# Performance work log

Hardware: AMD Instinct MI355X
Metric: run time of the kernel (lower is better)

Reference implementation:

```python
import jax, jax.numpy as jnp
import numpy as np

N = 50000
E = 1600000
IN_DIM = 128
HID = 32
HEADS = 4
OUT = 32
NEG_SLOPE = 0.2


def gat_conv(h, src, dst, W, al, ar, b, n_heads, d_out):
    # h: [N, F_in]; W: [F_in, H*D]; al/ar: [H, D]; b: [H*D]
    n = h.shape[0]
    z = (h @ W).reshape(n, n_heads, d_out)            # [N,H,D]
    el = (z * al[None]).sum(-1)                        # [N,H]
    er = (z * ar[None]).sum(-1)                        # [N,H]
    e = el[src] + er[dst]                              # [E,H]
    e = jnp.where(e > 0, e, NEG_SLOPE * e)             # leaky_relu(0.2)
    # edge softmax grouped by destination node
    m = jax.ops.segment_max(e, dst, num_segments=n)    # [N,H]
    ex = jnp.exp(e - m[dst])                           # [E,H]
    s = jax.ops.segment_sum(ex, dst, num_segments=n)   # [N,H]
    alpha = ex / s[dst]                                # [E,H]
    msg = alpha[:, :, None] * z[src]                   # [E,H,D]
    out = jax.ops.segment_sum(msg, dst, num_segments=n)  # [N,H,D]
    return out + b.reshape(1, n_heads, d_out)


def setup_inputs() -> dict:
    key = jax.random.key(0)
    ks = jax.random.split(key, 12)
    h = jax.random.normal(ks[0], (N, IN_DIM), dtype=jnp.float32)
    src = jax.random.randint(ks[1], (E,), 0, N, dtype=jnp.int32)
    dst = jax.random.randint(ks[2], (E,), 0, N, dtype=jnp.int32)
    s1 = 1.0 / np.sqrt(IN_DIM)
    W1 = jax.random.uniform(ks[3], (IN_DIM, HEADS * HID), jnp.float32, -s1, s1)
    al1 = jax.random.normal(ks[4], (HEADS, HID), jnp.float32) * 0.1
    ar1 = jax.random.normal(ks[5], (HEADS, HID), jnp.float32) * 0.1
    b1 = jnp.zeros((HEADS * HID,), jnp.float32)
    f2 = HEADS * HID
    s2 = 1.0 / np.sqrt(f2)
    W2 = jax.random.uniform(ks[6], (f2, OUT), jnp.float32, -s2, s2)
    al2 = jax.random.normal(ks[7], (1, OUT), jnp.float32) * 0.1
    ar2 = jax.random.normal(ks[8], (1, OUT), jnp.float32) * 0.1
    b2 = jnp.zeros((OUT,), jnp.float32)
    return {"h": h, "src": src, "dst": dst, "W1": W1, "al1": al1, "ar1": ar1,
            "b1": b1, "W2": W2, "al2": al2, "ar2": ar2, "b2": b2}


def reference(h, src, dst, W1, al1, ar1, b1, W2, al2, ar2, b2):
    x = gat_conv(h, src, dst, W1, al1, ar1, b1, HEADS, HID)  # [N,H,D]
    x = x.reshape(N, HEADS * HID)                             # flatten(1)
    x = jax.nn.elu(x)                                         # act
    y = gat_conv(x, src, dst, W2, al2, ar2, b2, 1, OUT)       # [N,1,OUT]
    return y.squeeze(1)                                        # [N,OUT]
```

## Files before the change

kernel.cpp:

```cpp
#include <hip/hip_runtime.h>
#include <hip/hip_fp16.h>

#define NN 50000
#define NEG_SLOPE 0.2f
#define BSHIFT 9
#define BNODES (1 << BSHIFT)
#define NBUCK ((NN + BNODES - 1) >> BSHIFT)
#define BCAP 18432

typedef _Float16 f16x4 __attribute__((ext_vector_type(4)));
typedef _Float16 f16x8 __attribute__((ext_vector_type(8)));
typedef float    f32x4 __attribute__((ext_vector_type(4)));

__global__ void zero_kernel(unsigned* bucket_cursor, int* src_sorted_pad) {
    int i = threadIdx.x;
    if (i < NBUCK) bucket_cursor[i] = (unsigned)(i * BCAP);
    if (i < 64) src_sorted_pad[i] = 0;
}

__global__ __launch_bounds__(1024) void bucketA(
        const int* __restrict__ src, const int* __restrict__ dst,
        unsigned* __restrict__ bucket_cursor, int2* __restrict__ ebuf, int E) {
    __shared__ unsigned hist[NBUCK];
    int tid = threadIdx.x;
    if (tid < NBUCK) hist[tid] = 0u;
    __syncthreads();
    int e = blockIdx.x * 1024 + tid;
    int s = 0, d = 0, b = 0;
    bool valid = e < E;
    if (valid) {
        s = src[e]; d = dst[e]; b = d >> BSHIFT;
        atomicAdd(&hist[b], 1u);
    }
    __syncthreads();
    if (tid < NBUCK) {
        unsigned c = hist[tid];
        hist[tid] = c ? atomicAdd(&bucket_cursor[tid], c) : 0u;
    }
    __syncthreads();
    if (valid) {
        unsigned slot = atomicAdd(&hist[b], 1u);
        ebuf[slot] = make_int2(s, d);
    }
}

__global__ __launch_bounds__(512) void gemm1_mfma(
        const float* __restrict__ h, const float* __restrict__ W1,
        const float* __restrict__ al1, const float* __restrict__ ar1,
        __half* __restrict__ z1h, float* __restrict__ el1, float* __restrict__ er1, int N) {
    __shared__ alignas(16) __half hA[128 * 128];
    __shared__ alignas(16) __half Bt[128 * 128];
    int tid = threadIdx.x;
    int lane = tid & 63, w = tid >> 6;
    int row0 = blockIdx.x * 128;
    int nrow = min(128, N - row0);

    for (int idx = tid; idx < 128 * 32; idx += 512) {
        int row = idx >> 5, kq = idx & 31;
        float4 v = (row < nrow) ? ((const float4*)(h + (size_t)(row0 + row) * 128))[kq]
                                : make_float4(0.f, 0.f, 0.f, 0.f);
        f16x4 hv;
        hv[0] = (_Float16)v.x; hv[1] = (_Float16)v.y;
        hv[2] = (_Float16)v.z; hv[3] = (_Float16)v.w;
        int off = row * 256 + ((kq * 8) ^ ((row & 15) << 4));
        *(f16x4*)((char*)hA + off) = hv;
    }
    {
        int col = tid & 127, kg = tid >> 7;
        #pragma unroll
        for (int it = 0; it < 4; ++it) {
            int k0 = it * 32 + kg * 8;
            f16x8 wv;
            #pragma unroll
            for (int i = 0; i < 8; ++i)
                wv[i] = (_Float16)W1[(size_t)(k0 + i) * 128 + col];
            int off = col * 256 + ((k0 * 2) ^ ((col & 15) << 4));
            *(f16x8*)((char*)Bt + off) = wv;
        }
    }
    __syncthreads();

    f32x4 acc[8];
    #pragma unroll
    for (int ct = 0; ct < 8; ++ct) acc[ct] = (f32x4){0.f, 0.f, 0.f, 0.f};

    int arow = w * 16 + (lane & 15);
    int kbyte_lane = ((lane >> 4) * 8) * 2;
    #pragma unroll
    for (int ks = 0; ks < 4; ++ks) {
        int kb = ks * 64 + kbyte_lane;
        f16x8 a = *(const f16x8*)((const char*)hA + arow * 256 + (kb ^ ((arow & 15) << 4)));
        #pragma unroll
        for (int ct = 0; ct < 8; ++ct) {
            int col = ct * 16 + (lane & 15);
            f16x8 b = *(const f16x8*)((const char*)Bt + col * 256 + (kb ^ ((col & 15) << 4)));
            acc[ct] = __builtin_amdgcn_mfma_f32_16x16x32_f16(a, b, acc[ct], 0, 0, 0);
        }
    }

    int lrow = (lane >> 4) * 4;
    #pragma unroll
    for (int ct = 0; ct < 8; ++ct) {
        int col = ct * 16 + (lane & 15);
        #pragma unroll
        for (int r = 0; r < 4; ++r) {
            int rl = w * 16 + lrow + r;
            if (rl < nrow)
                z1h[(size_t)(row0 + rl) * 128 + col] = __float2half(acc[ct][r]);
        }
    }
    #pragma unroll
    for (int hh = 0; hh < 4; ++hh) {
        int c0 = hh * 32 + (lane & 15);
        float a_l0 = al1[c0], a_l1 = al1[c0 + 16];
        float a_r0 = ar1[c0], a_r1 = ar1[c0 + 16];
        #pragma unroll
        for (int r = 0; r < 4; ++r) {
            float v0 = acc[2 * hh][r], v1 = acc[2 * hh + 1][r];
            float pl = v0 * a_l0 + v1 * a_l1;
            float pr = v0 * a_r0 + v1 * a_r1;
            #pragma unroll
            for (int o = 8; o; o >>= 1) {
                pl += __shfl_xor(pl, o, 16);
                pr += __shfl_xor(pr, o, 16);
            }
            int rl = w * 16 + lrow + r;
            if ((lane & 15) == 0 && rl < nrow) {
                el1[(row0 + rl) * 4 + hh] = pl;
                er1[(row0 + rl) * 4 + hh] = pr;
            }
        }
    }
}

__global__ __launch_bounds__(1024) void scatterC(
        const int2* __restrict__ ebuf, const unsigned* __restrict__ bucket_cursor,
        unsigned* __restrict__ off, int* __restrict__ src_sorted, int N, int E) {
    __shared__ unsigned hist[BNODES], nodeoff[BNODES], wsum[8], bsz[128];
    int b = blockIdx.x, tid = threadIdx.x;
    int base = b << BSHIFT;
    unsigned rs = (unsigned)(b * BCAP), re = bucket_cursor[b];

    if (tid < 128) bsz[tid] = (tid < NBUCK) ? bucket_cursor[tid] - (unsigned)(tid * BCAP) : 0u;
    if (tid < BNODES) hist[tid] = 0u;
    __syncthreads();
    if (tid == 0) {
        unsigned r = 0;
        for (int t = 0; t < NBUCK; ++t) { unsigned c = bsz[t]; bsz[t] = r; r += c; }
        if (b == 0) off[N] = (unsigned)E;
    }
    __syncthreads();
    unsigned boff = bsz[b];

    for (unsigned i = rs + tid; i < re; i += 1024)
        atomicAdd(&hist[ebuf[i].y - base], 1u);
    __syncthreads();
    unsigned v = 0, x = 0;
    int lane = tid & 63, wv = tid >> 6;
    if (tid < BNODES) {
        v = hist[tid]; x = v;
        #pragma unroll
        for (int o = 1; o < 64; o <<= 1) {
            unsigned n = __shfl_up(x, o, 64);
            if (lane >= o) x += n;
        }
        if (lane == 63) wsum[wv] = x;
    }
    __syncthreads();
    if (tid == 0) {
        unsigned r = 0;
        #pragma unroll
        for (int k = 0; k < 8; ++k) { unsigned t = wsum[k]; wsum[k] = r; r += t; }
    }
    __syncthreads();
    if (tid < BNODES) {
        unsigned exoff = x - v + wsum[wv] + boff;
        nodeoff[tid] = exoff;
        if (base + tid < N) off[base + tid] = exoff;
        hist[tid] = 0u;
    }
    __syncthreads();
    for (unsigned i = rs + tid; i < re; i += 1024) {
        int2 ed = ebuf[i];
        int ln = ed.y - base;
        unsigned r = atomicAdd(&hist[ln], 1u);
        src_sorted[nodeoff[ln] + r] = ed.x;
    }
}

__global__ __launch_bounds__(256) void agg1_spmm(
        const int* __restrict__ src_sorted, const unsigned* __restrict__ off,
        const float* __restrict__ el1, const float* __restrict__ er1,
        const __half* __restrict__ z1h, const float* __restrict__ b1, __half* __restrict__ x) {
    int tid = threadIdx.x, lane = tid & 63, w = tid >> 6;
    int node = blockIdx.x * 4 + w;
    int start = (int)off[node], end = (int)off[node + 1];
    int g = lane >> 4, l16 = lane & 15, head = l16 >> 2;
    const char* zbase = (const char*)z1h + (unsigned)(l16 * 16);
    float er_d = er1[node * 4 + head];

    float acc[8];
    #pragma unroll
    for (int jj = 0; jj < 8; ++jj) acc[jj] = 0.f;
    float sloc = 0.f;
    for (int base = start; base < end; base += 32) {
        #pragma unroll
        for (int t = 0; t < 8; ++t) {
            int i = base + 4 * t + g;
            int s = src_sorted[i];
            float el = el1[(unsigned)s * 4u + head];
            float v = el + er_d;
            v = fmaxf(v, NEG_SLOPE * v);
            float ex = __expf(v);
            ex = (i < end) ? ex : 0.f;
            sloc += ex;
            float4 r = *(const float4*)(zbase + ((unsigned)s << 8));
            const __half* zh = (const __half*)&r;
            #pragma unroll
            for (int k = 0; k < 8; ++k)
                acc[k] = fmaf(__half2float(zh[k]), ex, acc[k]);
        }
    }
    #pragma unroll
    for (int jj = 0; jj < 8; ++jj) {
        acc[jj] += __shfl_xor(acc[jj], 16, 64);
        acc[jj] += __shfl_xor(acc[jj], 32, 64);
    }
    sloc += __shfl_xor(sloc, 16, 64);
    sloc += __shfl_xor(sloc, 32, 64);
    float inv = sloc > 0.f ? 1.f / sloc : 0.f;

    if (g == 0) {
        float xv[8];
        #pragma unroll
        for (int jj = 0; jj < 8; ++jj) {
            float t = acc[jj] * inv + b1[l16 * 8 + jj];
            xv[jj] = t > 0.f ? t : (__expf(t) - 1.f);
        }
        union { __half2 h2[4]; uint4 u; } pk;
        #pragma unroll
        for (int k = 0; k < 4; ++k) pk.h2[k] = __floats2half2_rn(xv[2 * k], xv[2 * k + 1]);
        *(uint4*)(x + ((size_t)node << 7) + l16 * 8) = pk.u;
    }
}

__global__ __launch_bounds__(256) void gemm2el_kernel(
        const __half* __restrict__ x, const float* __restrict__ W2,
        const float* __restrict__ al2, const float* __restrict__ ar2,
        __half* __restrict__ z2h, float* __restrict__ el2, float* __restrict__ er2, int N) {
    __shared__ __half xsh[64][136];
    __shared__ float W2T[32][132];
    int tid = threadIdx.x;
    int row0 = blockIdx.x * 64;
    int nrow = min(64, N - row0);

    for (int idx = tid; idx < nrow * 16; idx += 256) {
        int r = idx >> 4, kq = idx & 15;
        float4 v = ((const float4*)(x + (size_t)(row0 + r) * 128))[kq];
        *(float4*)&xsh[r][kq * 8] = v;
    }
    for (int idx = tid; idx < 4096; idx += 256) {
        int k = idx >> 5, c = idx & 31;
        W2T[c][k] = W2[idx];
    }
    __syncthreads();

    int gc = tid & 15, gr = tid >> 4;
    float acc[4][2];
    #pragma unroll
    for (int j = 0; j < 4; ++j) { acc[j][0] = 0.f; acc[j][1] = 0.f; }

    for (int p = 0; p < 32; ++p) {
        float4 w0 = *(const float4*)&W2T[gc][p * 4];
        float4 w1 = *(const float4*)&W2T[gc + 16][p * 4];
        #pragma unroll
        for (int j = 0; j < 4; ++j) {
            const __half* xr = &xsh[gr * 4 + j][p * 4];
            float x0 = __half2float(xr[0]), x1 = __half2float(xr[1]);
            float x2 = __half2float(xr[2]), x3 = __half2float(xr[3]);
            acc[j][0] = fmaf(x0, w0.x, fmaf(x1, w0.y, fmaf(x2, w0.z, fmaf(x3, w0.w, acc[j][0]))));
            acc[j][1] = fmaf(x0, w1.x, fmaf(x1, w1.y, fmaf(x2, w1.z, fmaf(x3, w1.w, acc[j][1]))));
        }
    }

    float al0 = al2[gc], al1v = al2[gc + 16];
    float ar0 = ar2[gc], ar1v = ar2[gc + 16];
    #pragma unroll
    for (int j = 0; j < 4; ++j) {
        int r = gr * 4 + j;
        int node = row0 + r;
        bool live = r < nrow;
        if (live) {
            z2h[(size_t)node * 32 + gc]      = __float2half(acc[j][0]);
            z2h[(size_t)node * 32 + gc + 16] = __float2half(acc[j][1]);
        }
        float pl = acc[j][0] * al0 + acc[j][1] * al1v;
        float pr = acc[j][0] * ar0 + acc[j][1] * ar1v;
        #pragma unroll
        for (int o = 8; o; o >>= 1) {
            pl += __shfl_xor(pl, o, 16);
            pr += __shfl_xor(pr, o, 16);
        }
        if (live && gc == 0) { el2[node] = pl; er2[node] = pr; }
    }
}

__global__ __launch_bounds__(256) void agg2_fused(
        const int* __restrict__ src_sorted, const unsigned* __restrict__ off,
        const float* __restrict__ el2, const float* __restrict__ er2,
        const __half* __restrict__ z2h, const float* __restrict__ b2,
        float* __restrict__ out) {
    int tid = threadIdx.x, lane = tid & 63;
    int node = blockIdx.x * 4 + (tid >> 6);
    int start = (int)off[node], end = (int)off[node + 1];
    float er_d = er2[node];

    int g = lane >> 2, l4 = lane & 3;
    const char* zbase = (const char*)z2h + (unsigned)(l4 * 16);
    float acc[8];
    #pragma unroll
    for (int jj = 0; jj < 8; ++jj) acc[jj] = 0.f;
    float sloc = 0.f;
    for (int base = start; base < end; base += 64) {
        #pragma unroll
        for (int t = 0; t < 4; ++t) {
            int i = base + 16 * t + g;
            int s = src_sorted[i];
            float v = el2[s] + er_d;
            v = fmaxf(v, NEG_SLOPE * v);
            float ex = __expf(v);
            ex = (i < end) ? ex : 0.f;
            sloc += ex;
            float4 r = *(const float4*)(zbase + ((unsigned)s << 6));
            const __half* zh = (const __half*)&r;
            #pragma unroll
            for (int k = 0; k < 8; ++k)
                acc[k] = fmaf(__half2float(zh[k]), ex, acc[k]);
        }
    }
    #pragma unroll
    for (int jj = 0; jj < 8; ++jj) {
        acc[jj] += __shfl_xor(acc[jj], 4, 64);
        acc[jj] += __shfl_xor(acc[jj], 8, 64);
        acc[jj] += __shfl_xor(acc[jj], 16, 64);
        acc[jj] += __shfl_xor(acc[jj], 32, 64);
    }
    sloc += __shfl_xor(sloc, 4, 64);
    sloc += __shfl_xor(sloc, 8, 64);
    sloc += __shfl_xor(sloc, 16, 64);
    sloc += __shfl_xor(sloc, 32, 64);
    float inv = sloc > 0.f ? 1.f / sloc : 0.f;
    if (g == 0) {
        #pragma unroll
        for (int jj = 0; jj < 8; ++jj)
            out[(size_t)node * 32 + l4 * 8 + jj] = acc[jj] * inv + b2[l4 * 8 + jj];
    }
}

extern "C" void kernel_launch(void* const* d_in, const int* in_sizes, int n_in,
                              void* d_out, int out_size, void* d_ws, size_t ws_size,
                              hipStream_t stream) {
    const float* h   = (const float*)d_in[0];
    const int*   src = (const int*)d_in[1];
    const int*   dst = (const int*)d_in[2];
    const float* W1  = (const float*)d_in[3];
    const float* al1 = (const float*)d_in[4];
    const float* ar1 = (const float*)d_in[5];
    const float* b1  = (const float*)d_in[6];
    const float* W2  = (const float*)d_in[7];
    const float* al2 = (const float*)d_in[8];
    const float* ar2 = (const float*)d_in[9];
    const float* b2  = (const float*)d_in[10];
    float* out = (float*)d_out;
    const int N = NN;
    const int E = in_sizes[1];

    char* w = (char*)d_ws;
    __half* z1h       = (__half*)w;   w += (size_t)N * 128 * 2;
    __half* z2h       = (__half*)w;   w += (size_t)N * 32 * 2;
    __half* xh        = (__half*)w;   w += (size_t)N * 128 * 2;
    int2*  ebuf       = (int2*)w;     w += (size_t)NBUCK * BCAP * 8;
    int*   src_sorted = (int*)w;      w += ((size_t)E + 64) * 4;
    float* el1        = (float*)w;    w += (size_t)N * 4 * 4;
    float* er1        = (float*)w;    w += (size_t)N * 4 * 4;
    float* el2        = (float*)w;    w += (size_t)N * 4;
    float* er2        = (float*)w;    w += (size_t)N * 4;
    unsigned* off     = (unsigned*)w; w += (size_t)(N + 16) * 4;
    unsigned* bucket_cursor = (unsigned*)w; w += 128 * 4;

    zero_kernel<<<1, 128, 0, stream>>>(bucket_cursor, src_sorted + E);
    bucketA<<<(E + 1023) / 1024, 1024, 0, stream>>>(src, dst, bucket_cursor, ebuf, E);
    gemm1_mfma<<<(N + 127) / 128, 512, 0, stream>>>(h, W1, al1, ar1, z1h, el1, er1, N);
    scatterC<<<NBUCK, 1024, 0, stream>>>(ebuf, bucket_cursor, off, src_sorted, N, E);
    agg1_spmm<<<N / 4, 256, 0, stream>>>(src_sorted, off, el1, er1, z1h, b1, xh);
    gemm2el_kernel<<<(N + 63) / 64, 256, 0, stream>>>(xh, W2, al2, ar2, z2h, el2, er2, N);
    agg2_fused<<<N / 4, 256, 0, stream>>>(src_sorted, off, el2, er2, z2h, b2, out);
}
```

Before: 267.6 us.

## Fuse layer-2 GEMM into layer-1 aggregation and pack edge buffer into 32 bits

Layer-1 aggregation now computes the ELU output into shared memory and immediately multiplies it by W2 to produce z2, el2 and er2 per node. This removes the fp16 x intermediate and the separate gemm2 kernel launch. In exchange, every 4-node block reloads the full 16KB W2 into shared memory and adds a block-wide barrier. Separately, edge buckets now pack src and the local dst into one 32-bit word, which halves ebuf traffic in the bucketing and scatter passes. The packing relies on src fitting in 23 bits.

```diff
diff --git a/kernel.cpp b/kernel.cpp
--- a/kernel.cpp
+++ b/kernel.cpp
@@ -20,7 +20,7 @@
 
 __global__ __launch_bounds__(1024) void bucketA(
         const int* __restrict__ src, const int* __restrict__ dst,
-        unsigned* __restrict__ bucket_cursor, int2* __restrict__ ebuf, int E) {
+        unsigned* __restrict__ bucket_cursor, unsigned* __restrict__ ebuf, int E) {
     __shared__ unsigned hist[NBUCK];
     int tid = threadIdx.x;
     if (tid < NBUCK) hist[tid] = 0u;
@@ -40,7 +40,7 @@
     __syncthreads();
     if (valid) {
         unsigned slot = atomicAdd(&hist[b], 1u);
-        ebuf[slot] = make_int2(s, d);
+        ebuf[slot] = ((unsigned)s << BSHIFT) | ((unsigned)d & (BNODES - 1));
     }
 }
 
@@ -134,7 +134,7 @@
 }
 
 __global__ __launch_bounds__(1024) void scatterC(
-        const int2* __restrict__ ebuf, const unsigned* __restrict__ bucket_cursor,
+        const unsigned* __restrict__ ebuf, const unsigned* __restrict__ bucket_cursor,
         unsigned* __restrict__ off, int* __restrict__ src_sorted, int N, int E) {
     __shared__ unsigned hist[BNODES], nodeoff[BNODES], wsum[8], bsz[128];
     int b = blockIdx.x, tid = threadIdx.x;
@@ -153,7 +153,7 @@
     unsigned boff = bsz[b];
 
     for (unsigned i = rs + tid; i < re; i += 1024)
-        atomicAdd(&hist[ebuf[i].y - base], 1u);
+        atomicAdd(&hist[ebuf[i] & (BNODES - 1u)], 1u);
     __syncthreads();
     unsigned v = 0, x = 0;
     int lane = tid & 63, wv = tid >> 6;
@@ -181,23 +181,33 @@
     }
     __syncthreads();
     for (unsigned i = rs + tid; i < re; i += 1024) {
-        int2 ed = ebuf[i];
-        int ln = ed.y - base;
+        unsigned pk = ebuf[i];
+        unsigned ln = pk & (BNODES - 1u);
         unsigned r = atomicAdd(&hist[ln], 1u);
-        src_sorted[nodeoff[ln] + r] = ed.x;
-    }
-}
-
-__global__ __launch_bounds__(256) void agg1_spmm(
+        src_sorted[nodeoff[ln] + r] = (int)(pk >> BSHIFT);
+    }
+}
+
+__global__ __launch_bounds__(256) void agg1_fused(
         const int* __restrict__ src_sorted, const unsigned* __restrict__ off,
         const float* __restrict__ el1, const float* __restrict__ er1,
-        const __half* __restrict__ z1h, const float* __restrict__ b1, __half* __restrict__ x) {
+        const __half* __restrict__ z1h, const float* __restrict__ b1,
+        const float* __restrict__ W2, const float* __restrict__ al2,
+        const float* __restrict__ ar2, __half* __restrict__ z2h,
+        float* __restrict__ el2, float* __restrict__ er2) {
+    __shared__ float W2s[32][132];
+    __shared__ float xrow[4][128];
     int tid = threadIdx.x, lane = tid & 63, w = tid >> 6;
     int node = blockIdx.x * 4 + w;
     int start = (int)off[node], end = (int)off[node + 1];
     int g = lane >> 4, l16 = lane & 15, head = l16 >> 2;
     const char* zbase = (const char*)z1h + (unsigned)(l16 * 16);
     float er_d = er1[node * 4 + head];
+
+    for (int idx = tid; idx < 4096; idx += 256) {
+        int k = idx >> 5, c = idx & 31;
+        W2s[c][k] = W2[idx];
+    }
 
     float acc[8];
     #pragma unroll
@@ -231,78 +241,33 @@
     float inv = sloc > 0.f ? 1.f / sloc : 0.f;
 
     if (g == 0) {
-        float xv[8];
         #pragma unroll
         for (int jj = 0; jj < 8; ++jj) {
             float t = acc[jj] * inv + b1[l16 * 8 + jj];
-            xv[jj] = t > 0.f ? t : (__expf(t) - 1.f);
-        }
-        union { __half2 h2[4]; uint4 u; } pk;
-        #pragma unroll
-        for (int k = 0; k < 4; ++k) pk.h2[k] = __floats2half2_rn(xv[2 * k], xv[2 * k + 1]);
-        *(uint4*)(x + ((size_t)node << 7) + l16 * 8) = pk.u;
-    }
-}
-
-__global__ __launch_bounds__(256) void gemm2el_kernel(
-        const __half* __restrict__ x, const float* __restrict__ W2,
-        const float* __restrict__ al2, const float* __restrict__ ar2,
-        __half* __restrict__ z2h, float* __restrict__ el2, float* __restrict__ er2, int N) {
-    __shared__ __half xsh[64][136];
-    __shared__ float W2T[32][132];
-    int tid = threadIdx.x;
-    int row0 = blockIdx.x * 64;
-    int nrow = min(64, N - row0);
-
-    for (int idx = tid; idx < nrow * 16; idx += 256) {
-        int r = idx >> 4, kq = idx & 15;
-        float4 v = ((const float4*)(x + (size_t)(row0 + r) * 128))[kq];
-        *(float4*)&xsh[r][kq * 8] = v;
-    }
-    for (int idx = tid; idx < 4096; idx += 256) {
-        int k = idx >> 5, c = idx & 31;
-        W2T[c][k] = W2[idx];
-    }
-    __syncthreads();
-
-    int gc = tid & 15, gr = tid >> 4;
-    float acc[4][2];
-    #pragma unroll
-    for (int j = 0; j < 4; ++j) { acc[j][0] = 0.f; acc[j][1] = 0.f; }
-
-    for (int p = 0; p < 32; ++p) {
-        float4 w0 = *(const float4*)&W2T[gc][p * 4];
-        float4 w1 = *(const float4*)&W2T[gc + 16][p * 4];
-        #pragma unroll
-        for (int j = 0; j < 4; ++j) {
-            const __half* xr = &xsh[gr * 4 + j][p * 4];
-            float x0 = __half2float(xr[0]), x1 = __half2float(xr[1]);
-            float x2 = __half2float(xr[2]), x3 = __half2float(xr[3]);
-            acc[j][0] = fmaf(x0, w0.x, fmaf(x1, w0.y, fmaf(x2, w0.z, fmaf(x3, w0.w, acc[j][0]))));
-            acc[j][1] = fmaf(x0, w1.x, fmaf(x1, w1.y, fmaf(x2, w1.z, fmaf(x3, w1.w, acc[j][1]))));
-        }
-    }
-
-    float al0 = al2[gc], al1v = al2[gc + 16];
-    float ar0 = ar2[gc], ar1v = ar2[gc + 16];
-    #pragma unroll
-    for (int j = 0; j < 4; ++j) {
-        int r = gr * 4 + j;
-        int node = row0 + r;
-        bool live = r < nrow;
-        if (live) {
-            z2h[(size_t)node * 32 + gc]      = __float2half(acc[j][0]);
-            z2h[(size_t)node * 32 + gc + 16] = __float2half(acc[j][1]);
-        }
-        float pl = acc[j][0] * al0 + acc[j][1] * al1v;
-        float pr = acc[j][0] * ar0 + acc[j][1] * ar1v;
-        #pragma unroll
-        for (int o = 8; o; o >>= 1) {
-            pl += __shfl_xor(pl, o, 16);
-            pr += __shfl_xor(pr, o, 16);
-        }
-        if (live && gc == 0) { el2[node] = pl; er2[node] = pr; }
-    }
+            xrow[w][l16 * 8 + jj] = t > 0.f ? t : (__expf(t) - 1.f);
+        }
+    }
+    __syncthreads();
+
+    int c = lane & 31, half = lane >> 5;
+    const float* xr = xrow[w];
+    float z2 = 0.f;
+    #pragma unroll
+    for (int kq = 0; kq < 16; ++kq) {
+        int k = half * 64 + kq * 4;
+        float4 wv = *(const float4*)&W2s[c][k];
+        float4 xv = *(const float4*)&xr[k];
+        z2 = fmaf(xv.x, wv.x, fmaf(xv.y, wv.y, fmaf(xv.z, wv.z, fmaf(xv.w, wv.w, z2))));
+    }
+    z2 += __shfl_xor(z2, 32, 64);
+    if (half == 0) z2h[(size_t)node * 32 + c] = __float2half(z2);
+    float pl = z2 * al2[c], pr = z2 * ar2[c];
+    #pragma unroll
+    for (int o = 16; o; o >>= 1) {
+        pl += __shfl_xor(pl, o, 32);
+        pr += __shfl_xor(pr, o, 32);
+    }
+    if (lane == 0) { el2[node] = pl; er2[node] = pr; }
 }
 
 __global__ __launch_bounds__(256) void agg2_fused(
@@ -378,8 +343,7 @@
     char* w = (char*)d_ws;
     __half* z1h       = (__half*)w;   w += (size_t)N * 128 * 2;
     __half* z2h       = (__half*)w;   w += (size_t)N * 32 * 2;
-    __half* xh        = (__half*)w;   w += (size_t)N * 128 * 2;
-    int2*  ebuf       = (int2*)w;     w += (size_t)NBUCK * BCAP * 8;
+    unsigned* ebuf    = (unsigned*)w; w += (size_t)NBUCK * BCAP * 4;
     int*   src_sorted = (int*)w;      w += ((size_t)E + 64) * 4;
     float* el1        = (float*)w;    w += (size_t)N * 4 * 4;
     float* er1        = (float*)w;    w += (size_t)N * 4 * 4;
@@ -392,7 +356,7 @@
     bucketA<<<(E + 1023) / 1024, 1024, 0, stream>>>(src, dst, bucket_cursor, ebuf, E);
     gemm1_mfma<<<(N + 127) / 128, 512, 0, stream>>>(h, W1, al1, ar1, z1h, el1, er1, N);
     scatterC<<<NBUCK, 1024, 0, stream>>>(ebuf, bucket_cursor, off, src_sorted, N, E);
-    agg1_spmm<<<N / 4, 256, 0, stream>>>(src_sorted, off, el1, er1, z1h, b1, xh);
-    gemm2el_kernel<<<(N + 63) / 64, 256, 0, stream>>>(xh, W2, al2, ar2, z2h, el2, er2, N);
+    agg1_fused<<<N / 4, 256, 0, stream>>>(src_sorted, off, el1, er1, z1h, b1,
+                                          W2, al2, ar2, z2h, el2, er2);
     agg2_fused<<<N / 4, 256, 0, stream>>>(src_sorted, off, el2, er2, z2h, b2, out);
 }
```

New measurement: 269.0 us. No clear change (+0.5%).
